# Performance work log

Hardware: AMD Instinct MI355X
Metric: run time of the kernel (lower is better)

## Reference

```python
import jax, jax.numpy as jnp
import numpy as np


def setup_inputs() -> dict:
    key = jax.random.key(0)
    k1, k2 = jax.random.split(key)
    B, C, H, W = 8, 256, 64, 64
    x = jax.random.normal(k1, (B, C, H, W), dtype=jnp.float32)
    # gamma is a learned scalar (nn.Parameter(torch.zeros(1))); init nonzero
    # so the attention branch contributes to the output for testing.
    gamma = jax.random.normal(k2, (1,), dtype=jnp.float32)
    return {"x": x, "gamma": gamma}


def reference(x, gamma):
    B, C, H, W = x.shape
    f = x.reshape(B, C, H * W)  # (B, C, N) with N = H*W
    # attn[b, n, m] = softmax_m( sum_c f[b,c,n] * f[b,c,m] )  -- no scaling, per module
    scores = jnp.einsum('bcn,bcm->bnm', f, f)  # (B, N, N)
    attn = jax.nn.softmax(scores, axis=-1)
    # out[b, c, n] = sum_m f[b,c,m] * attn[b,n,m]   (bmm(d, attn^T))
    out = jnp.einsum('bcm,bnm->bcn', f, attn).reshape(B, C, H, W)
    return gamma * out + x
```

## Files before the change

kernel.cpp:

```cpp
#include <hip/hip_runtime.h>
#include <hip/hip_bf16.h>

typedef __attribute__((ext_vector_type(8))) short short8;
typedef __attribute__((ext_vector_type(4))) float f32x4;
typedef __attribute__((ext_vector_type(16))) float f32x16;
typedef __attribute__((ext_vector_type(4))) unsigned int u32x4;

#define NB 8
#define NC 256
#define NNN 4096
#define L2E 1.44269504088896f

__device__ __forceinline__ ushort f2bf(float f) {
  __hip_bfloat16 h = __float2bfloat16(f);
  return *reinterpret_cast<ushort*>(&h);
}
__device__ __forceinline__ unsigned pack2(float a, float b) {
  return (unsigned)f2bf(a) | ((unsigned)f2bf(b) << 16);
}
__device__ __forceinline__ void gload16(const void* g, void* l) {
  __builtin_amdgcn_global_load_lds(
      (const __attribute__((address_space(1))) void*)g,
      (__attribute__((address_space(3))) void*)l, 16, 0, 0);
}

__global__ __launch_bounds__(256) void prep_T(const float* __restrict__ x,
                                              ushort* __restrict__ fTs) {
  __shared__ float tile[32][33];
  const int tx = threadIdx.x, ty = threadIdx.y;
  const int n0 = blockIdx.x * 32, c0 = blockIdx.y * 32, b = blockIdx.z;
#pragma unroll
  for (int k = 0; k < 4; ++k) {
    tile[ty + 8 * k][tx] =
        x[((size_t)(b * NC + c0 + ty + 8 * k)) * NNN + n0 + tx];
  }
  __syncthreads();
#pragma unroll
  for (int k = 0; k < 4; ++k) {
    const int n = n0 + ty + 8 * k;
    const int c = c0 + tx;
    fTs[(size_t)(b * NNN + n) * NC + (c ^ ((n & 7) << 3))] =
        f2bf(tile[tx][ty + 8 * k]);
  }
}

__global__ __launch_bounds__(256) void prep_V(const float* __restrict__ x,
                                              ushort* __restrict__ fVs) {
  const size_t ci = (size_t)blockIdx.x * 256 + threadIdx.x;
  const int p = (int)(ci & 511);
  const int c = (int)((ci >> 9) & 255);
  const int b = (int)(ci >> 17);
  const int lp = (p & ~7) | ((p & 7) ^ (c & 7));
  const float* src = x + ((size_t)(b * NC + c)) * NNN + lp * 8;
  f32x4 a0 = *(const f32x4*)src;
  f32x4 a1 = *(const f32x4*)(src + 4);
  short8 w;
  w[0] = (short)f2bf(a0[0]); w[1] = (short)f2bf(a0[1]);
  w[2] = (short)f2bf(a0[2]); w[3] = (short)f2bf(a0[3]);
  w[4] = (short)f2bf(a1[0]); w[5] = (short)f2bf(a1[1]);
  w[6] = (short)f2bf(a1[2]); w[7] = (short)f2bf(a1[3]);
  *(short8*)(fVs + ((size_t)(b * NC + c)) * NNN + p * 8) = w;
}

__global__ __launch_bounds__(256, 1) void attn_kernel(
    const float* __restrict__ x, const ushort* __restrict__ fTs,
    const ushort* __restrict__ fVs, const float* __restrict__ gamma,
    float* __restrict__ out) {
  __shared__ __align__(16) char smem[131072];

  const int tid = threadIdx.x;
  const int w = tid >> 6;
  const int l = tid & 63;
  const int l31 = l & 31;
  const int h = l >> 5;
  const int b = blockIdx.x & 7;
  const int gn0 = (blockIdx.x >> 3) * 128;
  const int n0w = gn0 + w * 32;

  const char* fTb = (const char*)(fTs + (size_t)b * NNN * NC);
  const char* fVb = (const char*)(fVs + (size_t)b * NNN * NC);

  short8 q[16];
  {
    const int n = n0w + l31;
    const char* qrow = fTb + (size_t)n * 512;
    const int sw = (n & 7) << 4;
#pragma unroll
    for (int kc = 0; kc < 16; ++kc)
      q[kc] = *(const short8*)(qrow + ((kc * 32 + 16 * h) ^ sw));
  }

  f32x16 o[8];
#pragma unroll
  for (int cf = 0; cf < 8; ++cf)
#pragma unroll
    for (int r = 0; r < 16; ++r) o[cf][r] = 0.f;
  float m_run = -3.0e38f, l_run = 0.f;

  const int krow = w * 16 + (l >> 5);
  const char* gK0 = fTb + (size_t)krow * 512 + (l & 31) * 16;
  const int vrow = w * 64 + (l >> 3);
  const char* gV0 = fVb + (size_t)vrow * 8192 + (l & 7) * 16;

#pragma unroll
  for (int i = 0; i < 8; ++i)
    gload16(gK0 + (size_t)i * 1024, smem + w * 8192 + i * 1024);
#pragma unroll
  for (int i = 0; i < 8; ++i)
    gload16(gV0 + (size_t)i * 65536, smem + 32768 + w * 8192 + i * 1024);
  __syncthreads();

  for (int t = 0; t < 64; ++t) {
    const int p = t & 1;
    char* bufC = smem + p * 65536;
    char* bufN = smem + (p ^ 1) * 65536;
    if (t < 63) {
      const size_t kOff = (size_t)(t + 1) * 64 * 512;
      const size_t vOff = (size_t)(t + 1) * 128;
#pragma unroll
      for (int i = 0; i < 8; ++i)
        gload16(gK0 + kOff + (size_t)i * 1024, bufN + w * 8192 + i * 1024);
#pragma unroll
      for (int i = 0; i < 8; ++i)
        gload16(gV0 + vOff + (size_t)i * 65536,
                bufN + 32768 + w * 8192 + i * 1024);
    }

    const char* Kp = bufC;
    const char* Vp = bufC + 32768;
    f32x16 s0, s1;
#pragma unroll
    for (int r = 0; r < 16; ++r) { s0[r] = 0.f; s1[r] = 0.f; }
#pragma unroll
    for (int kc = 0; kc < 16; ++kc) {
      const int bb = (kc * 32 + 16 * h) ^ ((l31 & 7) << 4);
      short8 ka0 = *(const short8*)(Kp + l31 * 512 + bb);
      short8 ka1 = *(const short8*)(Kp + (32 + l31) * 512 + bb);
      s0 = __builtin_amdgcn_mfma_f32_32x32x16_bf16(ka0, q[kc], s0, 0, 0, 0);
      s1 = __builtin_amdgcn_mfma_f32_32x32x16_bf16(ka1, q[kc], s1, 0, 0, 0);
    }

    float tm = s0[0];
#pragma unroll
    for (int r = 1; r < 16; ++r) tm = fmaxf(tm, s0[r]);
#pragma unroll
    for (int r = 0; r < 16; ++r) tm = fmaxf(tm, s1[r]);
    tm = fmaxf(tm, __shfl_xor(tm, 32));

    if (__any(tm > m_run + 8.f)) {
      const float mnew = fmaxf(m_run, tm);
      const float alpha = exp2f((m_run - mnew) * L2E);
      m_run = mnew;
      l_run *= alpha;
      float ar[16];
#pragma unroll
      for (int r = 0; r < 16; ++r)
        ar[r] = __shfl(alpha, (r & 3) + 8 * (r >> 2) + 4 * h);
#pragma unroll
      for (int cf = 0; cf < 8; ++cf)
#pragma unroll
        for (int r = 0; r < 16; ++r) o[cf][r] *= ar[r];
    }

    float rsum = 0.f;
#pragma unroll
    for (int r = 0; r < 16; ++r) {
      float pv = exp2f((s0[r] - m_run) * L2E); s0[r] = pv; rsum += pv;
    }
#pragma unroll
    for (int r = 0; r < 16; ++r) {
      float pv = exp2f((s1[r] - m_run) * L2E); s1[r] = pv; rsum += pv;
    }
    rsum += __shfl_xor(rsum, 32);
    l_run += rsum;

    unsigned d0[8], d1[8];
#pragma unroll
    for (int k = 0; k < 8; ++k) {
      const int rg = 4 * (k >> 1) + 2 * (k & 1);
      d0[k] = pack2(s0[rg], s0[rg + 1]);
      d1[k] = pack2(s1[rg], s1[rg + 1]);
    }
    unsigned x0[4], x1[4];
#pragma unroll
    for (int j = 0; j < 4; ++j) {
      const int iH1 = (j < 2) ? j : j + 2;
      const int iH0 = (j < 2) ? j + 2 : j + 4;
      unsigned s0v = h ? d0[iH1] : d0[iH0];
      unsigned s1v = h ? d1[iH1] : d1[iH0];
      x0[j] = (unsigned)__shfl_xor((int)s0v, 32);
      x1[j] = (unsigned)__shfl_xor((int)s1v, 32);
    }

#pragma unroll
    for (int ks = 0; ks < 4; ++ks) {
      const int e = ks & 1;
      unsigned fa0, fa1, fa2, fa3;
      if (ks < 2) {
        fa0 = h ? x0[2 * e] : d0[4 * e];
        fa1 = h ? x0[2 * e + 1] : d0[4 * e + 1];
        fa2 = h ? d0[4 * e + 2] : x0[2 * e];
        fa3 = h ? d0[4 * e + 3] : x0[2 * e + 1];
      } else {
        fa0 = h ? x1[2 * e] : d1[4 * e];
        fa1 = h ? x1[2 * e + 1] : d1[4 * e + 1];
        fa2 = h ? d1[4 * e + 2] : x1[2 * e];
        fa3 = h ? d1[4 * e + 3] : x1[2 * e + 1];
      }
      u32x4 fu = {fa0, fa1, fa2, fa3};
      short8 pa = __builtin_bit_cast(short8, fu);
#pragma unroll
      for (int cf = 0; cf < 8; ++cf) {
        const int c = cf * 32 + l31;
        const int byte = (ks * 32 + 16 * h) ^ ((c & 7) << 4);
        short8 vb = *(const short8*)(Vp + c * 128 + byte);
        o[cf] = __builtin_amdgcn_mfma_f32_32x32x16_bf16(pa, vb, o[cf], 0, 0, 0);
      }
    }
    __syncthreads();
  }

  const float linv = 1.0f / l_run;
  float lr[16];
#pragma unroll
  for (int r = 0; r < 16; ++r)
    lr[r] = __shfl(linv, (r & 3) + 8 * (r >> 2) + 4 * h);
  const float gam = gamma[0];
  float* ot = (float*)smem + w * (32 * 129);
#pragma unroll
  for (int pass = 0; pass < 2; ++pass) {
#pragma unroll
    for (int cf = 0; cf < 4; ++cf) {
      const int cfg = pass * 4 + cf;
#pragma unroll
      for (int r = 0; r < 16; ++r) {
        const int nr = (r & 3) + 8 * (r >> 2) + 4 * h;
        ot[nr * 129 + cf * 32 + l31] = o[cfg][r] * lr[r];
      }
    }
    __syncthreads();
#pragma unroll 8
    for (int i = 0; i < 64; ++i) {
      const int cl = 2 * i + h;
      const float ov = ot[l31 * 129 + cl];
      const size_t gi =
          ((size_t)(b * NC + pass * 128 + cl)) * NNN + n0w + l31;
      out[gi] = gam * ov + x[gi];
    }
    __syncthreads();
  }
}

extern "C" void kernel_launch(void* const* d_in, const int* in_sizes, int n_in,
                              void* d_out, int out_size, void* d_ws,
                              size_t ws_size, hipStream_t stream) {
  const float* x = (const float*)d_in[0];
  const float* gamma = (const float*)d_in[1];
  float* out = (float*)d_out;
  ushort* fTs = (ushort*)d_ws;
  ushort* fVs = (ushort*)d_ws + (size_t)NB * NNN * NC;

  dim3 pg(NNN / 32, NC / 32, NB);
  dim3 pb(32, 8, 1);
  prep_T<<<pg, pb, 0, stream>>>(x, fTs);
  prep_V<<<dim3(4096), dim3(256), 0, stream>>>(x, fVs);

  attn_kernel<<<dim3(256), dim3(256), 0, stream>>>(x, fTs, fVs, gamma, out);
}
```

Before: 245.2 us.

## Split each query tile across two waves along key dimension with 512-thread blocks

Doubles the block to 8 waves. Each pair of waves shares a 32-query tile and splits every 64-key chunk, with one wave taking 32 keys each. Row maxima are exchanged through LDS with a barrier every iteration, and partial outputs and denominators are merged through shared memory at the end. The output MFMA is transposed (V as the A operand, P as B) so rescaling uses a per-lane scalar and needs no shuffles. This aims to raise latency hiding and MFMA issue parallelism. In exchange it adds an extra workgroup barrier per iteration, and the launch_bounds(512,2) with ~129KB LDS cannot actually fit two blocks per CU.

New measurement: 367.8 us. 1.5x slower.

```diff
diff --git a/kernel.cpp b/kernel.cpp
--- a/kernel.cpp
+++ b/kernel.cpp
@@ -62,20 +62,23 @@
   *(short8*)(fVs + ((size_t)(b * NC + c)) * NNN + p * 8) = w;
 }
 
-__global__ __launch_bounds__(256, 1) void attn_kernel(
+__global__ __launch_bounds__(512, 2) void attn_kernel(
     const float* __restrict__ x, const ushort* __restrict__ fTs,
     const ushort* __restrict__ fVs, const float* __restrict__ gamma,
     float* __restrict__ out) {
-  __shared__ __align__(16) char smem[131072];
+  __shared__ __align__(16) char smem[132096];
+  float* stats = (float*)(smem + 131072);
 
   const int tid = threadIdx.x;
-  const int w = tid >> 6;
+  const int w8 = tid >> 6;
+  const int g = w8 >> 1;
+  const int mh = w8 & 1;
   const int l = tid & 63;
   const int l31 = l & 31;
   const int h = l >> 5;
   const int b = blockIdx.x & 7;
   const int gn0 = (blockIdx.x >> 3) * 128;
-  const int n0w = gn0 + w * 32;
+  const int n0w = gn0 + g * 32;
 
   const char* fTb = (const char*)(fTs + (size_t)b * NNN * NC);
   const char* fVb = (const char*)(fVs + (size_t)b * NNN * NC);
@@ -84,7 +87,7 @@
   {
     const int n = n0w + l31;
     const char* qrow = fTb + (size_t)n * 512;
-    const int sw = (n & 7) << 4;
+    const int sw = (l31 & 7) << 4;
 #pragma unroll
     for (int kc = 0; kc < 16; ++kc)
       q[kc] = *(const short8*)(qrow + ((kc * 32 + 16 * h) ^ sw));
@@ -95,159 +98,133 @@
   for (int cf = 0; cf < 8; ++cf)
 #pragma unroll
     for (int r = 0; r < 16; ++r) o[cf][r] = 0.f;
-  float m_run = -3.0e38f, l_run = 0.f;
-
-  const int krow = w * 16 + (l >> 5);
-  const char* gK0 = fTb + (size_t)krow * 512 + (l & 31) * 16;
-  const int vrow = w * 64 + (l >> 3);
-  const char* gV0 = fVb + (size_t)vrow * 8192 + (l & 7) * 16;
-
-#pragma unroll
-  for (int i = 0; i < 8; ++i)
-    gload16(gK0 + (size_t)i * 1024, smem + w * 8192 + i * 1024);
-#pragma unroll
-  for (int i = 0; i < 8; ++i)
-    gload16(gV0 + (size_t)i * 65536, smem + 32768 + w * 8192 + i * 1024);
+  float m_run = -3.0e38f, l_half = 0.f;
+
+  const char* kSrc = fTb + tid * 16;
+  const char* vSrc = fVb + (size_t)(l >> 3) * 8192 + (l & 7) * 16;
+  const int dstW = w8 << 10;
+
+#pragma unroll
+  for (int i = 0; i < 4; ++i)
+    gload16(kSrc + i * 8192, smem + dstW + i * 8192);
+#pragma unroll
+  for (int i = 0; i < 4; ++i)
+    gload16(vSrc + (size_t)(i * 8 + w8) * 65536, smem + 32768 + dstW + i * 8192);
   __syncthreads();
 
+  const int krow = mh * 32 + l31;
+  const int ksw = (l31 & 7) << 4;
+
   for (int t = 0; t < 64; ++t) {
-    const int p = t & 1;
-    char* bufC = smem + p * 65536;
-    char* bufN = smem + (p ^ 1) * 65536;
+    char* bufC = smem + (t & 1) * 65536;
     if (t < 63) {
-      const size_t kOff = (size_t)(t + 1) * 64 * 512;
+      char* bufN = smem + ((t + 1) & 1) * 65536;
+      const size_t kOff = (size_t)(t + 1) * 32768;
       const size_t vOff = (size_t)(t + 1) * 128;
 #pragma unroll
-      for (int i = 0; i < 8; ++i)
-        gload16(gK0 + kOff + (size_t)i * 1024, bufN + w * 8192 + i * 1024);
-#pragma unroll
-      for (int i = 0; i < 8; ++i)
-        gload16(gV0 + vOff + (size_t)i * 65536,
-                bufN + 32768 + w * 8192 + i * 1024);
-    }
-
-    const char* Kp = bufC;
-    const char* Vp = bufC + 32768;
-    f32x16 s0, s1;
-#pragma unroll
-    for (int r = 0; r < 16; ++r) { s0[r] = 0.f; s1[r] = 0.f; }
+      for (int i = 0; i < 4; ++i)
+        gload16(kSrc + kOff + i * 8192, bufN + dstW + i * 8192);
+#pragma unroll
+      for (int i = 0; i < 4; ++i)
+        gload16(vSrc + (size_t)(i * 8 + w8) * 65536 + vOff,
+                bufN + 32768 + dstW + i * 8192);
+    }
+
+    f32x16 s;
+#pragma unroll
+    for (int r = 0; r < 16; ++r) s[r] = 0.f;
 #pragma unroll
     for (int kc = 0; kc < 16; ++kc) {
-      const int bb = (kc * 32 + 16 * h) ^ ((l31 & 7) << 4);
-      short8 ka0 = *(const short8*)(Kp + l31 * 512 + bb);
-      short8 ka1 = *(const short8*)(Kp + (32 + l31) * 512 + bb);
-      s0 = __builtin_amdgcn_mfma_f32_32x32x16_bf16(ka0, q[kc], s0, 0, 0, 0);
-      s1 = __builtin_amdgcn_mfma_f32_32x32x16_bf16(ka1, q[kc], s1, 0, 0, 0);
-    }
-
-    float tm = s0[0];
-#pragma unroll
-    for (int r = 1; r < 16; ++r) tm = fmaxf(tm, s0[r]);
-#pragma unroll
-    for (int r = 0; r < 16; ++r) tm = fmaxf(tm, s1[r]);
+      short8 ka =
+          *(const short8*)(bufC + krow * 512 + ((kc * 32 + 16 * h) ^ ksw));
+      s = __builtin_amdgcn_mfma_f32_32x32x16_bf16(ka, q[kc], s, 0, 0, 0);
+    }
+
+    float tm = s[0];
+#pragma unroll
+    for (int r = 1; r < 16; ++r) tm = fmaxf(tm, s[r]);
     tm = fmaxf(tm, __shfl_xor(tm, 32));
-
-    if (__any(tm > m_run + 8.f)) {
-      const float mnew = fmaxf(m_run, tm);
+    stats[w8 * 32 + l31] = tm;
+    __builtin_amdgcn_sched_barrier(0);
+    asm volatile("s_waitcnt lgkmcnt(0)" ::: "memory");
+    __builtin_amdgcn_s_barrier();
+    __builtin_amdgcn_sched_barrier(0);
+    const float pm = stats[(w8 * 32 + l31) ^ 32];
+    const float mc = fmaxf(tm, pm);
+
+    if (__any(mc > m_run + 8.f)) {
+      const float mnew = fmaxf(m_run, mc);
       const float alpha = exp2f((m_run - mnew) * L2E);
       m_run = mnew;
-      l_run *= alpha;
-      float ar[16];
-#pragma unroll
-      for (int r = 0; r < 16; ++r)
-        ar[r] = __shfl(alpha, (r & 3) + 8 * (r >> 2) + 4 * h);
+      l_half *= alpha;
 #pragma unroll
       for (int cf = 0; cf < 8; ++cf)
 #pragma unroll
-        for (int r = 0; r < 16; ++r) o[cf][r] *= ar[r];
+        for (int r = 0; r < 16; ++r) o[cf][r] *= alpha;
     }
 
     float rsum = 0.f;
 #pragma unroll
     for (int r = 0; r < 16; ++r) {
-      float pv = exp2f((s0[r] - m_run) * L2E); s0[r] = pv; rsum += pv;
-    }
-#pragma unroll
-    for (int r = 0; r < 16; ++r) {
-      float pv = exp2f((s1[r] - m_run) * L2E); s1[r] = pv; rsum += pv;
+      const float pv = exp2f((s[r] - m_run) * L2E);
+      s[r] = pv;
+      rsum += pv;
     }
     rsum += __shfl_xor(rsum, 32);
-    l_run += rsum;
-
-    unsigned d0[8], d1[8];
-#pragma unroll
-    for (int k = 0; k < 8; ++k) {
-      const int rg = 4 * (k >> 1) + 2 * (k & 1);
-      d0[k] = pack2(s0[rg], s0[rg + 1]);
-      d1[k] = pack2(s1[rg], s1[rg + 1]);
-    }
-    unsigned x0[4], x1[4];
-#pragma unroll
-    for (int j = 0; j < 4; ++j) {
-      const int iH1 = (j < 2) ? j : j + 2;
-      const int iH0 = (j < 2) ? j + 2 : j + 4;
-      unsigned s0v = h ? d0[iH1] : d0[iH0];
-      unsigned s1v = h ? d1[iH1] : d1[iH0];
-      x0[j] = (unsigned)__shfl_xor((int)s0v, 32);
-      x1[j] = (unsigned)__shfl_xor((int)s1v, 32);
-    }
-
-#pragma unroll
-    for (int ks = 0; ks < 4; ++ks) {
-      const int e = ks & 1;
-      unsigned fa0, fa1, fa2, fa3;
-      if (ks < 2) {
-        fa0 = h ? x0[2 * e] : d0[4 * e];
-        fa1 = h ? x0[2 * e + 1] : d0[4 * e + 1];
-        fa2 = h ? d0[4 * e + 2] : x0[2 * e];
-        fa3 = h ? d0[4 * e + 3] : x0[2 * e + 1];
-      } else {
-        fa0 = h ? x1[2 * e] : d1[4 * e];
-        fa1 = h ? x1[2 * e + 1] : d1[4 * e + 1];
-        fa2 = h ? d1[4 * e + 2] : x1[2 * e];
-        fa3 = h ? d1[4 * e + 3] : x1[2 * e + 1];
-      }
-      u32x4 fu = {fa0, fa1, fa2, fa3};
-      short8 pa = __builtin_bit_cast(short8, fu);
+    l_half += rsum;
+
+    const char* Vp = bufC + 32768;
+#pragma unroll
+    for (int ks = 0; ks < 2; ++ks) {
+      const int ok = 8 * ks + 4 * h;
+      const int os = 8 * ks + 4 * (1 - h);
+      const unsigned uA = pack2(s[ok], s[ok + 1]);
+      const unsigned uB = pack2(s[ok + 2], s[ok + 3]);
+      const unsigned vA = pack2(s[os], s[os + 1]);
+      const unsigned vB = pack2(s[os + 2], s[os + 3]);
+      const unsigned xA = (unsigned)__shfl_xor((int)vA, 32);
+      const unsigned xB = (unsigned)__shfl_xor((int)vB, 32);
+      u32x4 fu;
+      if (h == 0) { fu[0] = uA; fu[1] = uB; fu[2] = xA; fu[3] = xB; }
+      else        { fu[0] = xA; fu[1] = xB; fu[2] = uA; fu[3] = uB; }
+      const short8 pb = __builtin_bit_cast(short8, fu);
+      const int mb = mh * 64 + ks * 32 + 16 * h;
 #pragma unroll
       for (int cf = 0; cf < 8; ++cf) {
         const int c = cf * 32 + l31;
-        const int byte = (ks * 32 + 16 * h) ^ ((c & 7) << 4);
-        short8 vb = *(const short8*)(Vp + c * 128 + byte);
-        o[cf] = __builtin_amdgcn_mfma_f32_32x32x16_bf16(pa, vb, o[cf], 0, 0, 0);
+        const short8 va =
+            *(const short8*)(Vp + c * 128 + (mb ^ ((c & 7) << 4)));
+        o[cf] = __builtin_amdgcn_mfma_f32_32x32x16_bf16(va, pb, o[cf], 0, 0, 0);
       }
     }
     __syncthreads();
   }
 
-  const float linv = 1.0f / l_run;
-  float lr[16];
-#pragma unroll
-  for (int r = 0; r < 16; ++r)
-    lr[r] = __shfl(linv, (r & 3) + 8 * (r >> 2) + 4 * h);
-  const float gam = gamma[0];
-  float* ot = (float*)smem + w * (32 * 129);
-#pragma unroll
-  for (int pass = 0; pass < 2; ++pass) {
-#pragma unroll
-    for (int cf = 0; cf < 4; ++cf) {
-      const int cfg = pass * 4 + cf;
+  stats[w8 * 32 + l31] = l_half;
+  if (mh == 1) {
+    float* Og = (float*)(smem + g * 32768);
+#pragma unroll
+    for (int cf = 0; cf < 8; ++cf)
 #pragma unroll
       for (int r = 0; r < 16; ++r) {
-        const int nr = (r & 3) + 8 * (r >> 2) + 4 * h;
-        ot[nr * 129 + cf * 32 + l31] = o[cfg][r] * lr[r];
+        const int c = cf * 32 + (r & 3) + 8 * (r >> 2) + 4 * h;
+        Og[c * 32 + l31] = o[cf][r];
       }
-    }
-    __syncthreads();
-#pragma unroll 8
-    for (int i = 0; i < 64; ++i) {
-      const int cl = 2 * i + h;
-      const float ov = ot[l31 * 129 + cl];
-      const size_t gi =
-          ((size_t)(b * NC + pass * 128 + cl)) * NNN + n0w + l31;
-      out[gi] = gam * ov + x[gi];
-    }
-    __syncthreads();
+  }
+  __syncthreads();
+  if (mh == 0) {
+    const float l_tot = stats[g * 64 + l31] + stats[g * 64 + 32 + l31];
+    const float sc = gamma[0] / l_tot;
+    const float* Og = (const float*)(smem + g * 32768);
+#pragma unroll
+    for (int cf = 0; cf < 8; ++cf)
+#pragma unroll
+      for (int r = 0; r < 16; ++r) {
+        const int c = cf * 32 + (r & 3) + 8 * (r >> 2) + 4 * h;
+        const float val = (o[cf][r] + Og[c * 32 + l31]) * sc;
+        const size_t gi = ((size_t)(b * NC + c)) * NNN + n0w + l31;
+        out[gi] = val + x[gi];
+      }
   }
 }
 
@@ -265,5 +242,5 @@
   prep_T<<<pg, pb, 0, stream>>>(x, fTs);
   prep_V<<<dim3(4096), dim3(256), 0, stream>>>(x, fVs);
 
-  attn_kernel<<<dim3(256), dim3(256), 0, stream>>>(x, fTs, fVs, gamma, out);
-}
+  attn_kernel<<<dim3(256), dim3(512), 0, stream>>>(x, fTs, fVs, gamma, out);
+}
```
